# Kernel tuning notes

Measured on AMD Instinct MI355X. Metric: run time of the kernel, lower is better.

Reference implementation:

```python
import jax, jax.numpy as jnp
import numpy as np

B, T, I, H, O = 512, 1024, 15, 64, 11

def setup_inputs() -> dict:
    key = jax.random.key(0)
    ks = jax.random.split(key, 7)
    s_ih = 1.0 / np.sqrt(H)
    return {
        "x": jax.random.normal(ks[0], (B, T, I), dtype=jnp.float32),
        # torch nn.RNN params: weight_ih_l0 [H,I], weight_hh_l0 [H,H], biases [H]
        "W_ih": jax.random.uniform(ks[1], (H, I), jnp.float32, -s_ih, s_ih),
        "b_ih": jax.random.uniform(ks[2], (H,), jnp.float32, -s_ih, s_ih),
        "W_hh": jax.random.uniform(ks[3], (H, H), jnp.float32, -s_ih, s_ih),
        "b_hh": jax.random.uniform(ks[4], (H,), jnp.float32, -s_ih, s_ih),
        # decoder Linear(64, 11)
        "W_dec": jax.random.uniform(ks[5], (O, H), jnp.float32, -s_ih, s_ih),
        "b_dec": jax.random.uniform(ks[6], (O,), jnp.float32, -s_ih, s_ih),
    }

def reference(x, W_ih, b_ih, W_hh, b_hh, W_dec, b_dec):
    # Precompute input projection for all timesteps: [T, B, H]
    xproj = jnp.einsum("bti,hi->tbh", x, W_ih) + b_ih + b_hh
    h0 = jnp.zeros((x.shape[0], W_hh.shape[0]), dtype=x.dtype)

    def step(h, xp_t):
        h_new = jax.nn.relu(xp_t + h @ W_hh.T)  # [B, H]
        return h_new, h_new

    h_last, hs = jax.lax.scan(step, h0, xproj)  # hs: [T, B, H]
    out_seq = jnp.transpose(hs, (1, 0, 2))       # [B, T, H]
    out = jax.nn.relu(jnp.einsum("bth,oh->bto", out_seq, W_dec) + b_dec)
    h = h_last[None]  # [1, B, H] matching torch num_layers dim
    return (out, h)
```

## Files before the change

### kernel.cpp

```cpp
#include <hip/hip_runtime.h>
#include <hip/hip_fp16.h>
#include <stdint.h>

#define BB 512
#define TT 1024
#define II 15
#define HH 64
#define OO 11

typedef __fp16 half2v __attribute__((ext_vector_type(2)));
typedef _Float16 half8 __attribute__((ext_vector_type(8)));
typedef float floatx4 __attribute__((ext_vector_type(4)));
typedef int int4v __attribute__((ext_vector_type(4)));

union PK { int i; half2v h; float f; };

__device__ __forceinline__ half2v i2h2(int v) { PK u; u.i = v; return u.h; }
__device__ __forceinline__ int h22i(half2v v) { PK u; u.h = v; return u.i; }

__device__ __forceinline__ float FDOT2(half2v a, half2v b, float c) {
    return __builtin_amdgcn_fdot2(a, b, c, false);
}

__global__ __launch_bounds__(64) void rnn_rec(
    const float* __restrict__ x, const float* __restrict__ W_ih,
    const float* __restrict__ b_ih, const float* __restrict__ W_hh,
    const float* __restrict__ b_hh, _Float16* __restrict__ hs,
    float* __restrict__ h_last)
{
    __shared__ __align__(16) int xbuf[2][64 * 8];
    __shared__ __align__(16) _Float16 hbuf[64];
    const int b = blockIdx.x;
    const int lane = threadIdx.x;

    half2v whh[32];
#pragma unroll
    for (int p = 0; p < 32; ++p)
        whh[p] = __builtin_amdgcn_cvt_pkrtz(W_hh[lane * HH + 2 * p],
                                            W_hh[lane * HH + 2 * p + 1]);
    half2v wx[8];
#pragma unroll
    for (int j = 0; j < 7; ++j)
        wx[j] = __builtin_amdgcn_cvt_pkrtz(W_ih[lane * II + 2 * j],
                                           W_ih[lane * II + 2 * j + 1]);
    wx[7] = __builtin_amdgcn_cvt_pkrtz(W_ih[lane * II + 14],
                                       b_ih[lane] + b_hh[lane]);

    const float* xb = x + (size_t)b * TT * II;
    _Float16* hrow = hs + (size_t)b * TT * HH + lane;
    const int4v* hb4 = (const int4v*)hbuf;

    {
        float cf[II];
#pragma unroll
        for (int i = 0; i < II; ++i) cf[i] = xb[lane * II + i];
        int4v p0, p1;
        p0.x = h22i(__builtin_amdgcn_cvt_pkrtz(cf[0], cf[1]));
        p0.y = h22i(__builtin_amdgcn_cvt_pkrtz(cf[2], cf[3]));
        p0.z = h22i(__builtin_amdgcn_cvt_pkrtz(cf[4], cf[5]));
        p0.w = h22i(__builtin_amdgcn_cvt_pkrtz(cf[6], cf[7]));
        p1.x = h22i(__builtin_amdgcn_cvt_pkrtz(cf[8], cf[9]));
        p1.y = h22i(__builtin_amdgcn_cvt_pkrtz(cf[10], cf[11]));
        p1.z = h22i(__builtin_amdgcn_cvt_pkrtz(cf[12], cf[13]));
        p1.w = h22i(__builtin_amdgcn_cvt_pkrtz(cf[14], 1.0f));
        *(int4v*)&xbuf[0][lane * 8] = p0;
        *(int4v*)&xbuf[0][lane * 8 + 4] = p1;
    }
    hbuf[lane] = (_Float16)0.0f;

    float xa[8];
    {
        const int4v xv0 = *(const int4v*)&xbuf[0][0];
        const int4v xv1 = *(const int4v*)&xbuf[0][4];
        xa[0] = FDOT2(i2h2(xv0.x), wx[0], 0.0f);
        xa[1] = FDOT2(i2h2(xv0.y), wx[1], 0.0f);
        xa[2] = FDOT2(i2h2(xv0.z), wx[2], 0.0f);
        xa[3] = FDOT2(i2h2(xv0.w), wx[3], 0.0f);
        xa[4] = FDOT2(i2h2(xv1.x), wx[4], 0.0f);
        xa[5] = FDOT2(i2h2(xv1.y), wx[5], 0.0f);
        xa[6] = FDOT2(i2h2(xv1.z), wx[6], 0.0f);
        xa[7] = FDOT2(i2h2(xv1.w), wx[7], 0.0f);
    }

    float h = 0.0f;

    auto step = [&](int t) {
        int4v hb[8];
#pragma unroll
        for (int q = 0; q < 8; ++q) hb[q] = hb4[q];

        const int tn = t + 1;
        const int* xp = &xbuf[(tn >> 6) & 1][(tn & 63) * 8];
        const int4v xv0 = *(const int4v*)xp;
        const int4v xv1 = *(const int4v*)(xp + 4);

        float a0 = xa[0], a1 = xa[1], a2 = xa[2], a3 = xa[3];
        float a4 = xa[4], a5 = xa[5], a6 = xa[6], a7 = xa[7];
#pragma unroll
        for (int r = 0; r < 4; ++r) {
            a0 = FDOT2(i2h2(hb[2 * r].x),     whh[8 * r + 0], a0);
            a1 = FDOT2(i2h2(hb[2 * r].y),     whh[8 * r + 1], a1);
            a2 = FDOT2(i2h2(hb[2 * r].z),     whh[8 * r + 2], a2);
            a3 = FDOT2(i2h2(hb[2 * r].w),     whh[8 * r + 3], a3);
            a4 = FDOT2(i2h2(hb[2 * r + 1].x), whh[8 * r + 4], a4);
            a5 = FDOT2(i2h2(hb[2 * r + 1].y), whh[8 * r + 5], a5);
            a6 = FDOT2(i2h2(hb[2 * r + 1].z), whh[8 * r + 6], a6);
            a7 = FDOT2(i2h2(hb[2 * r + 1].w), whh[8 * r + 7], a7);
        }
        h = fmaxf(((a0 + a1) + (a2 + a3)) + ((a4 + a5) + (a6 + a7)), 0.0f);
        const _Float16 hf = (_Float16)h;
        hbuf[lane] = hf;
        hrow[(size_t)t * HH] = hf;

        xa[0] = FDOT2(i2h2(xv0.x), wx[0], 0.0f);
        xa[1] = FDOT2(i2h2(xv0.y), wx[1], 0.0f);
        xa[2] = FDOT2(i2h2(xv0.z), wx[2], 0.0f);
        xa[3] = FDOT2(i2h2(xv0.w), wx[3], 0.0f);
        xa[4] = FDOT2(i2h2(xv1.x), wx[4], 0.0f);
        xa[5] = FDOT2(i2h2(xv1.y), wx[5], 0.0f);
        xa[6] = FDOT2(i2h2(xv1.z), wx[6], 0.0f);
        xa[7] = FDOT2(i2h2(xv1.w), wx[7], 0.0f);
    };

    for (int tc = 0; tc < TT; tc += 64) {
        const int tnb = (tc + 64 < TT) ? (tc + 64) : tc;
        float nf[II];
#pragma unroll
        for (int i = 0; i < II; ++i)
            nf[i] = xb[(size_t)(tnb + lane) * II + i];

        for (int to = 0; to < 32; to += 8)
#pragma unroll
            for (int u = 0; u < 8; ++u) step(tc + to + u);

        {
            const int cb = ((tc >> 6) + 1) & 1;
            int4v p0, p1;
            p0.x = h22i(__builtin_amdgcn_cvt_pkrtz(nf[0], nf[1]));
            p0.y = h22i(__builtin_amdgcn_cvt_pkrtz(nf[2], nf[3]));
            p0.z = h22i(__builtin_amdgcn_cvt_pkrtz(nf[4], nf[5]));
            p0.w = h22i(__builtin_amdgcn_cvt_pkrtz(nf[6], nf[7]));
            p1.x = h22i(__builtin_amdgcn_cvt_pkrtz(nf[8], nf[9]));
            p1.y = h22i(__builtin_amdgcn_cvt_pkrtz(nf[10], nf[11]));
            p1.z = h22i(__builtin_amdgcn_cvt_pkrtz(nf[12], nf[13]));
            p1.w = h22i(__builtin_amdgcn_cvt_pkrtz(nf[14], 1.0f));
            *(int4v*)&xbuf[cb][lane * 8] = p0;
            *(int4v*)&xbuf[cb][lane * 8 + 4] = p1;
        }

        for (int to = 32; to < 64; to += 8)
#pragma unroll
            for (int u = 0; u < 8; ++u) step(tc + to + u);
    }
    h_last[b * HH + lane] = h;
}

__global__ __launch_bounds__(256) void rnn_decode(
    const _Float16* __restrict__ hs, const float* __restrict__ W_dec,
    const float* __restrict__ b_dec, float* __restrict__ out)
{
    __shared__ __align__(16) _Float16 wl[16 * HH];
    const int tid = threadIdx.x;
    for (int i = tid; i < 16 * HH; i += 256)
        wl[i] = (_Float16)((i < OO * HH) ? W_dec[i] : 0.0f);
    __syncthreads();

    const int lane = tid & 63;
    const int wid  = tid >> 6;
    const int col  = lane & 15;
    const int quad = lane >> 4;
    const float bd = (col < OO) ? b_dec[col] : 0.0f;

    half8 bf0 = *(const half8*)&wl[col * HH + quad * 8];
    half8 bf1 = *(const half8*)&wl[col * HH + 32 + quad * 8];

    const size_t tile = (size_t)blockIdx.x * 4 + wid;
    const size_t btb = tile * 16;
    const _Float16* ap = hs + (btb + (size_t)col) * HH + quad * 8;
    half8 a0 = *(const half8*)ap;
    half8 a1 = *(const half8*)(ap + 32);

    floatx4 acc = {0.0f, 0.0f, 0.0f, 0.0f};
    acc = __builtin_amdgcn_mfma_f32_16x16x32_f16(a0, bf0, acc, 0, 0, 0);
    acc = __builtin_amdgcn_mfma_f32_16x16x32_f16(a1, bf1, acc, 0, 0, 0);

    if (col < OO) {
#pragma unroll
        for (int r = 0; r < 4; ++r) {
            const size_t row = btb + (size_t)(quad * 4 + r);
            out[row * OO + col] = fmaxf(acc[r] + bd, 0.0f);
        }
    }
}

extern "C" void kernel_launch(void* const* d_in, const int* in_sizes, int n_in,
                              void* d_out, int out_size, void* d_ws, size_t ws_size,
                              hipStream_t stream) {
    const float* x     = (const float*)d_in[0];
    const float* W_ih  = (const float*)d_in[1];
    const float* b_ih  = (const float*)d_in[2];
    const float* W_hh  = (const float*)d_in[3];
    const float* b_hh  = (const float*)d_in[4];
    const float* W_dec = (const float*)d_in[5];
    const float* b_dec = (const float*)d_in[6];

    float* out    = (float*)d_out;
    float* h_last = out + (size_t)BB * TT * OO;
    _Float16* hs  = (_Float16*)d_ws;

    rnn_rec<<<BB, 64, 0, stream>>>(x, W_ih, b_ih, W_hh, b_hh, hs, h_last);
    rnn_decode<<<8192, 256, 0, stream>>>(hs, W_dec, b_dec, out);
}
```

Measured before the change: 273.8 us.

## Pack two batch rows per wavefront, each lane computing two hidden units

Each 64-lane block now handles two batch sequences: lanes 0-31 and 32-63 each own one batch, and every lane computes two hidden outputs with twice the recurrent weights held in registers. The grid is halved to 256 blocks, and hidden state is exchanged and stored as packed half2 words. This doubles per-lane serial work per step but halves the number of wavefronts, which suits a GPU with fewer CUs than 512 blocks, and it also doubles register pressure.

```diff
diff --git a/kernel.cpp b/kernel.cpp
--- a/kernel.cpp
+++ b/kernel.cpp
@@ -28,106 +28,143 @@
     const float* __restrict__ b_hh, _Float16* __restrict__ hs,
     float* __restrict__ h_last)
 {
-    __shared__ __align__(16) int xbuf[2][64 * 8];
-    __shared__ __align__(16) _Float16 hbuf[64];
-    const int b = blockIdx.x;
+    __shared__ __align__(16) int xbuf[2][2][64 * 8];
+    __shared__ __align__(16) int hbuf[64];
     const int lane = threadIdx.x;
-
-    half2v whh[32];
-#pragma unroll
-    for (int p = 0; p < 32; ++p)
-        whh[p] = __builtin_amdgcn_cvt_pkrtz(W_hh[lane * HH + 2 * p],
-                                            W_hh[lane * HH + 2 * p + 1]);
-    half2v wx[8];
-#pragma unroll
-    for (int j = 0; j < 7; ++j)
-        wx[j] = __builtin_amdgcn_cvt_pkrtz(W_ih[lane * II + 2 * j],
-                                           W_ih[lane * II + 2 * j + 1]);
-    wx[7] = __builtin_amdgcn_cvt_pkrtz(W_ih[lane * II + 14],
-                                       b_ih[lane] + b_hh[lane]);
-
-    const float* xb = x + (size_t)b * TT * II;
-    _Float16* hrow = hs + (size_t)b * TT * HH + lane;
-    const int4v* hb4 = (const int4v*)hbuf;
+    const int half = lane >> 5;
+    const int c = lane & 31;
+    const int b = blockIdx.x * 2 + half;
+    const int o0 = 2 * c, o1 = 2 * c + 1;
+
+    half2v wh0[32], wh1[32];
+#pragma unroll
+    for (int p = 0; p < 32; ++p) {
+        wh0[p] = __builtin_amdgcn_cvt_pkrtz(W_hh[o0 * HH + 2 * p],
+                                            W_hh[o0 * HH + 2 * p + 1]);
+        wh1[p] = __builtin_amdgcn_cvt_pkrtz(W_hh[o1 * HH + 2 * p],
+                                            W_hh[o1 * HH + 2 * p + 1]);
+    }
+    half2v wx0[8], wx1[8];
+#pragma unroll
+    for (int j = 0; j < 7; ++j) {
+        wx0[j] = __builtin_amdgcn_cvt_pkrtz(W_ih[o0 * II + 2 * j],
+                                            W_ih[o0 * II + 2 * j + 1]);
+        wx1[j] = __builtin_amdgcn_cvt_pkrtz(W_ih[o1 * II + 2 * j],
+                                            W_ih[o1 * II + 2 * j + 1]);
+    }
+    wx0[7] = __builtin_amdgcn_cvt_pkrtz(W_ih[o0 * II + 14],
+                                        b_ih[o0] + b_hh[o0]);
+    wx1[7] = __builtin_amdgcn_cvt_pkrtz(W_ih[o1 * II + 14],
+                                        b_ih[o1] + b_hh[o1]);
+
+    const float* xb0 = x + (size_t)(blockIdx.x * 2) * TT * II;
+    const float* xb1 = x + (size_t)(blockIdx.x * 2 + 1) * TT * II;
+    int* hrow = (int*)(hs + (size_t)b * TT * HH) + c;
 
     {
-        float cf[II];
-#pragma unroll
-        for (int i = 0; i < II; ++i) cf[i] = xb[lane * II + i];
-        int4v p0, p1;
-        p0.x = h22i(__builtin_amdgcn_cvt_pkrtz(cf[0], cf[1]));
-        p0.y = h22i(__builtin_amdgcn_cvt_pkrtz(cf[2], cf[3]));
-        p0.z = h22i(__builtin_amdgcn_cvt_pkrtz(cf[4], cf[5]));
-        p0.w = h22i(__builtin_amdgcn_cvt_pkrtz(cf[6], cf[7]));
-        p1.x = h22i(__builtin_amdgcn_cvt_pkrtz(cf[8], cf[9]));
-        p1.y = h22i(__builtin_amdgcn_cvt_pkrtz(cf[10], cf[11]));
-        p1.z = h22i(__builtin_amdgcn_cvt_pkrtz(cf[12], cf[13]));
-        p1.w = h22i(__builtin_amdgcn_cvt_pkrtz(cf[14], 1.0f));
-        *(int4v*)&xbuf[0][lane * 8] = p0;
-        *(int4v*)&xbuf[0][lane * 8 + 4] = p1;
-    }
-    hbuf[lane] = (_Float16)0.0f;
-
-    float xa[8];
+#pragma unroll
+        for (int q = 0; q < 2; ++q) {
+            const float* xq = q ? xb1 : xb0;
+            float cf[II];
+#pragma unroll
+            for (int i = 0; i < II; ++i) cf[i] = xq[lane * II + i];
+            int4v p0, p1;
+            p0.x = h22i(__builtin_amdgcn_cvt_pkrtz(cf[0], cf[1]));
+            p0.y = h22i(__builtin_amdgcn_cvt_pkrtz(cf[2], cf[3]));
+            p0.z = h22i(__builtin_amdgcn_cvt_pkrtz(cf[4], cf[5]));
+            p0.w = h22i(__builtin_amdgcn_cvt_pkrtz(cf[6], cf[7]));
+            p1.x = h22i(__builtin_amdgcn_cvt_pkrtz(cf[8], cf[9]));
+            p1.y = h22i(__builtin_amdgcn_cvt_pkrtz(cf[10], cf[11]));
+            p1.z = h22i(__builtin_amdgcn_cvt_pkrtz(cf[12], cf[13]));
+            p1.w = h22i(__builtin_amdgcn_cvt_pkrtz(cf[14], 1.0f));
+            *(int4v*)&xbuf[q][0][lane * 8] = p0;
+            *(int4v*)&xbuf[q][0][lane * 8 + 4] = p1;
+        }
+    }
+    hbuf[lane] = 0;
+
+    float xa0[4], xa1[4];
     {
-        const int4v xv0 = *(const int4v*)&xbuf[0][0];
-        const int4v xv1 = *(const int4v*)&xbuf[0][4];
-        xa[0] = FDOT2(i2h2(xv0.x), wx[0], 0.0f);
-        xa[1] = FDOT2(i2h2(xv0.y), wx[1], 0.0f);
-        xa[2] = FDOT2(i2h2(xv0.z), wx[2], 0.0f);
-        xa[3] = FDOT2(i2h2(xv0.w), wx[3], 0.0f);
-        xa[4] = FDOT2(i2h2(xv1.x), wx[4], 0.0f);
-        xa[5] = FDOT2(i2h2(xv1.y), wx[5], 0.0f);
-        xa[6] = FDOT2(i2h2(xv1.z), wx[6], 0.0f);
-        xa[7] = FDOT2(i2h2(xv1.w), wx[7], 0.0f);
-    }
-
-    float h = 0.0f;
+        const int4v xv0 = *(const int4v*)&xbuf[half][0][0];
+        const int4v xv1 = *(const int4v*)&xbuf[half][0][4];
+        xa0[0] = FDOT2(i2h2(xv0.x), wx0[0], 0.0f);
+        xa0[1] = FDOT2(i2h2(xv0.y), wx0[1], 0.0f);
+        xa0[2] = FDOT2(i2h2(xv0.z), wx0[2], 0.0f);
+        xa0[3] = FDOT2(i2h2(xv0.w), wx0[3], 0.0f);
+        xa0[0] = FDOT2(i2h2(xv1.x), wx0[4], xa0[0]);
+        xa0[1] = FDOT2(i2h2(xv1.y), wx0[5], xa0[1]);
+        xa0[2] = FDOT2(i2h2(xv1.z), wx0[6], xa0[2]);
+        xa0[3] = FDOT2(i2h2(xv1.w), wx0[7], xa0[3]);
+        xa1[0] = FDOT2(i2h2(xv0.x), wx1[0], 0.0f);
+        xa1[1] = FDOT2(i2h2(xv0.y), wx1[1], 0.0f);
+        xa1[2] = FDOT2(i2h2(xv0.z), wx1[2], 0.0f);
+        xa1[3] = FDOT2(i2h2(xv0.w), wx1[3], 0.0f);
+        xa1[0] = FDOT2(i2h2(xv1.x), wx1[4], xa1[0]);
+        xa1[1] = FDOT2(i2h2(xv1.y), wx1[5], xa1[1]);
+        xa1[2] = FDOT2(i2h2(xv1.z), wx1[6], xa1[2]);
+        xa1[3] = FDOT2(i2h2(xv1.w), wx1[7], xa1[3]);
+    }
+
+    float h0 = 0.0f, h1 = 0.0f;
 
     auto step = [&](int t) {
         int4v hb[8];
 #pragma unroll
-        for (int q = 0; q < 8; ++q) hb[q] = hb4[q];
+        for (int q = 0; q < 8; ++q)
+            hb[q] = *(const int4v*)&hbuf[half * 32 + q * 4];
+
+        float A0 = xa0[0], A1 = xa0[1], A2 = xa0[2], A3 = xa0[3];
+        float B0 = xa1[0], B1 = xa1[1], B2 = xa1[2], B3 = xa1[3];
+#pragma unroll
+        for (int q = 0; q < 8; ++q) {
+            A0 = FDOT2(i2h2(hb[q].x), wh0[4 * q + 0], A0);
+            A1 = FDOT2(i2h2(hb[q].y), wh0[4 * q + 1], A1);
+            A2 = FDOT2(i2h2(hb[q].z), wh0[4 * q + 2], A2);
+            A3 = FDOT2(i2h2(hb[q].w), wh0[4 * q + 3], A3);
+            B0 = FDOT2(i2h2(hb[q].x), wh1[4 * q + 0], B0);
+            B1 = FDOT2(i2h2(hb[q].y), wh1[4 * q + 1], B1);
+            B2 = FDOT2(i2h2(hb[q].z), wh1[4 * q + 2], B2);
+            B3 = FDOT2(i2h2(hb[q].w), wh1[4 * q + 3], B3);
+        }
+        h0 = fmaxf((A0 + A1) + (A2 + A3), 0.0f);
+        h1 = fmaxf((B0 + B1) + (B2 + B3), 0.0f);
+        const int pk = h22i(__builtin_amdgcn_cvt_pkrtz(h0, h1));
+        hbuf[half * 32 + c] = pk;
 
         const int tn = t + 1;
-        const int* xp = &xbuf[(tn >> 6) & 1][(tn & 63) * 8];
+        const int* xp = &xbuf[half][(tn >> 6) & 1][(tn & 63) * 8];
         const int4v xv0 = *(const int4v*)xp;
         const int4v xv1 = *(const int4v*)(xp + 4);
 
-        float a0 = xa[0], a1 = xa[1], a2 = xa[2], a3 = xa[3];
-        float a4 = xa[4], a5 = xa[5], a6 = xa[6], a7 = xa[7];
-#pragma unroll
-        for (int r = 0; r < 4; ++r) {
-            a0 = FDOT2(i2h2(hb[2 * r].x),     whh[8 * r + 0], a0);
-            a1 = FDOT2(i2h2(hb[2 * r].y),     whh[8 * r + 1], a1);
-            a2 = FDOT2(i2h2(hb[2 * r].z),     whh[8 * r + 2], a2);
-            a3 = FDOT2(i2h2(hb[2 * r].w),     whh[8 * r + 3], a3);
-            a4 = FDOT2(i2h2(hb[2 * r + 1].x), whh[8 * r + 4], a4);
-            a5 = FDOT2(i2h2(hb[2 * r + 1].y), whh[8 * r + 5], a5);
-            a6 = FDOT2(i2h2(hb[2 * r + 1].z), whh[8 * r + 6], a6);
-            a7 = FDOT2(i2h2(hb[2 * r + 1].w), whh[8 * r + 7], a7);
-        }
-        h = fmaxf(((a0 + a1) + (a2 + a3)) + ((a4 + a5) + (a6 + a7)), 0.0f);
-        const _Float16 hf = (_Float16)h;
-        hbuf[lane] = hf;
-        hrow[(size_t)t * HH] = hf;
-
-        xa[0] = FDOT2(i2h2(xv0.x), wx[0], 0.0f);
-        xa[1] = FDOT2(i2h2(xv0.y), wx[1], 0.0f);
-        xa[2] = FDOT2(i2h2(xv0.z), wx[2], 0.0f);
-        xa[3] = FDOT2(i2h2(xv0.w), wx[3], 0.0f);
-        xa[4] = FDOT2(i2h2(xv1.x), wx[4], 0.0f);
-        xa[5] = FDOT2(i2h2(xv1.y), wx[5], 0.0f);
-        xa[6] = FDOT2(i2h2(xv1.z), wx[6], 0.0f);
-        xa[7] = FDOT2(i2h2(xv1.w), wx[7], 0.0f);
+        hrow[(size_t)t * 32] = pk;
+
+        xa0[0] = FDOT2(i2h2(xv0.x), wx0[0], 0.0f);
+        xa0[1] = FDOT2(i2h2(xv0.y), wx0[1], 0.0f);
+        xa0[2] = FDOT2(i2h2(xv0.z), wx0[2], 0.0f);
+        xa0[3] = FDOT2(i2h2(xv0.w), wx0[3], 0.0f);
+        xa0[0] = FDOT2(i2h2(xv1.x), wx0[4], xa0[0]);
+        xa0[1] = FDOT2(i2h2(xv1.y), wx0[5], xa0[1]);
+        xa0[2] = FDOT2(i2h2(xv1.z), wx0[6], xa0[2]);
+        xa0[3] = FDOT2(i2h2(xv1.w), wx0[7], xa0[3]);
+        xa1[0] = FDOT2(i2h2(xv0.x), wx1[0], 0.0f);
+        xa1[1] = FDOT2(i2h2(xv0.y), wx1[1], 0.0f);
+        xa1[2] = FDOT2(i2h2(xv0.z), wx1[2], 0.0f);
+        xa1[3] = FDOT2(i2h2(xv0.w), wx1[3], 0.0f);
+        xa1[0] = FDOT2(i2h2(xv1.x), wx1[4], xa1[0]);
+        xa1[1] = FDOT2(i2h2(xv1.y), wx1[5], xa1[1]);
+        xa1[2] = FDOT2(i2h2(xv1.z), wx1[6], xa1[2]);
+        xa1[3] = FDOT2(i2h2(xv1.w), wx1[7], xa1[3]);
     };
 
     for (int tc = 0; tc < TT; tc += 64) {
         const int tnb = (tc + 64 < TT) ? (tc + 64) : tc;
-        float nf[II];
+        float nf0[II], nf1[II];
 #pragma unroll
         for (int i = 0; i < II; ++i)
-            nf[i] = xb[(size_t)(tnb + lane) * II + i];
+            nf0[i] = xb0[(size_t)(tnb + lane) * II + i];
+#pragma unroll
+        for (int i = 0; i < II; ++i)
+            nf1[i] = xb1[(size_t)(tnb + lane) * II + i];
 
         for (int to = 0; to < 32; to += 8)
 #pragma unroll
@@ -135,24 +172,29 @@
 
         {
             const int cb = ((tc >> 6) + 1) & 1;
-            int4v p0, p1;
-            p0.x = h22i(__builtin_amdgcn_cvt_pkrtz(nf[0], nf[1]));
-            p0.y = h22i(__builtin_amdgcn_cvt_pkrtz(nf[2], nf[3]));
-            p0.z = h22i(__builtin_amdgcn_cvt_pkrtz(nf[4], nf[5]));
-            p0.w = h22i(__builtin_amdgcn_cvt_pkrtz(nf[6], nf[7]));
-            p1.x = h22i(__builtin_amdgcn_cvt_pkrtz(nf[8], nf[9]));
-            p1.y = h22i(__builtin_amdgcn_cvt_pkrtz(nf[10], nf[11]));
-            p1.z = h22i(__builtin_amdgcn_cvt_pkrtz(nf[12], nf[13]));
-            p1.w = h22i(__builtin_amdgcn_cvt_pkrtz(nf[14], 1.0f));
-            *(int4v*)&xbuf[cb][lane * 8] = p0;
-            *(int4v*)&xbuf[cb][lane * 8 + 4] = p1;
+#pragma unroll
+            for (int q = 0; q < 2; ++q) {
+                const float* nf = q ? nf1 : nf0;
+                int4v p0, p1;
+                p0.x = h22i(__builtin_amdgcn_cvt_pkrtz(nf[0], nf[1]));
+                p0.y = h22i(__builtin_amdgcn_cvt_pkrtz(nf[2], nf[3]));
+                p0.z = h22i(__builtin_amdgcn_cvt_pkrtz(nf[4], nf[5]));
+                p0.w = h22i(__builtin_amdgcn_cvt_pkrtz(nf[6], nf[7]));
+                p1.x = h22i(__builtin_amdgcn_cvt_pkrtz(nf[8], nf[9]));
+                p1.y = h22i(__builtin_amdgcn_cvt_pkrtz(nf[10], nf[11]));
+                p1.z = h22i(__builtin_amdgcn_cvt_pkrtz(nf[12], nf[13]));
+                p1.w = h22i(__builtin_amdgcn_cvt_pkrtz(nf[14], 1.0f));
+                *(int4v*)&xbuf[q][cb][lane * 8] = p0;
+                *(int4v*)&xbuf[q][cb][lane * 8 + 4] = p1;
+            }
         }
 
         for (int to = 32; to < 64; to += 8)
 #pragma unroll
             for (int u = 0; u < 8; ++u) step(tc + to + u);
     }
-    h_last[b * HH + lane] = h;
+    h_last[(size_t)b * HH + o0] = h0;
+    h_last[(size_t)b * HH + o1] = h1;
 }
 
 __global__ __launch_bounds__(256) void rnn_decode(
@@ -208,6 +250,6 @@
     float* h_last = out + (size_t)BB * TT * OO;
     _Float16* hs  = (_Float16*)d_ws;
 
-    rnn_rec<<<BB, 64, 0, stream>>>(x, W_ih, b_ih, W_hh, b_hh, hs, h_last);
+    rnn_rec<<<BB / 2, 64, 0, stream>>>(x, W_ih, b_ih, W_hh, b_hh, hs, h_last);
     rnn_decode<<<8192, 256, 0, stream>>>(hs, W_dec, b_dec, out);
 }
```

New measurement: 346.3 us. 1.26x slower.

## Interleave two batch recurrences per wavefront to hide step latency

Applied to the files above, without the earlier changes.

Each 64-lane block now advances two independent batch rows in lockstep, alternating phases of the recurrence so that one row's LDS round-trip and dot-product chain overlaps with the other's. The grid is halved so that each wave carries two recurrences instead of one. The input-projection dot products move to the start of each phase, and the h reload is issued right after the write. In exchange it uses more registers per wave and fewer waves in total, so latency hiding now relies on interleaving within a wave rather than across waves.

```diff
diff --git a/kernel.cpp b/kernel.cpp
--- a/kernel.cpp
+++ b/kernel.cpp
@@ -28,10 +28,10 @@
     const float* __restrict__ b_hh, _Float16* __restrict__ hs,
     float* __restrict__ h_last)
 {
-    __shared__ __align__(16) int xbuf[2][64 * 8];
-    __shared__ __align__(16) _Float16 hbuf[64];
-    const int b = blockIdx.x;
+    __shared__ __align__(16) int xbuf[2][2][64 * 8];
+    __shared__ __align__(16) _Float16 hbuf[2][64];
     const int lane = threadIdx.x;
+    const int b0 = blockIdx.x * 2;
 
     half2v whh[32];
 #pragma unroll
@@ -46,14 +46,17 @@
     wx[7] = __builtin_amdgcn_cvt_pkrtz(W_ih[lane * II + 14],
                                        b_ih[lane] + b_hh[lane]);
 
-    const float* xb = x + (size_t)b * TT * II;
-    _Float16* hrow = hs + (size_t)b * TT * HH + lane;
-    const int4v* hb4 = (const int4v*)hbuf;
-
-    {
+    const float* xb0 = x + (size_t)b0 * TT * II;
+    const float* xb1 = x + (size_t)(b0 + 1) * TT * II;
+    _Float16* hr0 = hs + (size_t)b0 * TT * HH + lane;
+    _Float16* hr1 = hs + (size_t)(b0 + 1) * TT * HH + lane;
+
+#pragma unroll
+    for (int q = 0; q < 2; ++q) {
+        const float* xq = q ? xb1 : xb0;
         float cf[II];
 #pragma unroll
-        for (int i = 0; i < II; ++i) cf[i] = xb[lane * II + i];
+        for (int i = 0; i < II; ++i) cf[i] = xq[lane * II + i];
         int4v p0, p1;
         p0.x = h22i(__builtin_amdgcn_cvt_pkrtz(cf[0], cf[1]));
         p0.y = h22i(__builtin_amdgcn_cvt_pkrtz(cf[2], cf[3]));
@@ -63,39 +66,34 @@
         p1.y = h22i(__builtin_amdgcn_cvt_pkrtz(cf[10], cf[11]));
         p1.z = h22i(__builtin_amdgcn_cvt_pkrtz(cf[12], cf[13]));
         p1.w = h22i(__builtin_amdgcn_cvt_pkrtz(cf[14], 1.0f));
-        *(int4v*)&xbuf[0][lane * 8] = p0;
-        *(int4v*)&xbuf[0][lane * 8 + 4] = p1;
+        *(int4v*)&xbuf[q][0][lane * 8] = p0;
+        *(int4v*)&xbuf[q][0][lane * 8 + 4] = p1;
     }
-    hbuf[lane] = (_Float16)0.0f;
-
-    float xa[8];
-    {
-        const int4v xv0 = *(const int4v*)&xbuf[0][0];
-        const int4v xv1 = *(const int4v*)&xbuf[0][4];
-        xa[0] = FDOT2(i2h2(xv0.x), wx[0], 0.0f);
-        xa[1] = FDOT2(i2h2(xv0.y), wx[1], 0.0f);
-        xa[2] = FDOT2(i2h2(xv0.z), wx[2], 0.0f);
-        xa[3] = FDOT2(i2h2(xv0.w), wx[3], 0.0f);
-        xa[4] = FDOT2(i2h2(xv1.x), wx[4], 0.0f);
-        xa[5] = FDOT2(i2h2(xv1.y), wx[5], 0.0f);
-        xa[6] = FDOT2(i2h2(xv1.z), wx[6], 0.0f);
-        xa[7] = FDOT2(i2h2(xv1.w), wx[7], 0.0f);
-    }
-
-    float h = 0.0f;
-
-    auto step = [&](int t) {
-        int4v hb[8];
-#pragma unroll
-        for (int q = 0; q < 8; ++q) hb[q] = hb4[q];
-
-        const int tn = t + 1;
-        const int* xp = &xbuf[(tn >> 6) & 1][(tn & 63) * 8];
-        const int4v xv0 = *(const int4v*)xp;
-        const int4v xv1 = *(const int4v*)(xp + 4);
-
-        float a0 = xa[0], a1 = xa[1], a2 = xa[2], a3 = xa[3];
-        float a4 = xa[4], a5 = xa[5], a6 = xa[6], a7 = xa[7];
+    hbuf[0][lane] = (_Float16)0.0f;
+    hbuf[1][lane] = (_Float16)0.0f;
+
+    int4v hbA[8], hbB[8], xvA0, xvA1, xvB0, xvB1;
+#pragma unroll
+    for (int i = 0; i < 8; ++i) hbA[i] = ((const int4v*)hbuf[0])[i];
+    xvA0 = *(const int4v*)&xbuf[0][0][0];
+    xvA1 = *(const int4v*)&xbuf[0][0][4];
+#pragma unroll
+    for (int i = 0; i < 8; ++i) hbB[i] = ((const int4v*)hbuf[1])[i];
+    xvB0 = *(const int4v*)&xbuf[1][0][0];
+    xvB1 = *(const int4v*)&xbuf[1][0][4];
+
+    float hA = 0.0f, hB = 0.0f;
+
+    auto phase = [&](int q, int4v (&hb)[8], int4v& xv0, int4v& xv1,
+                     float& h, _Float16* hr, int t) {
+        float a0 = FDOT2(i2h2(xv0.x), wx[0], 0.0f);
+        float a1 = FDOT2(i2h2(xv0.y), wx[1], 0.0f);
+        float a2 = FDOT2(i2h2(xv0.z), wx[2], 0.0f);
+        float a3 = FDOT2(i2h2(xv0.w), wx[3], 0.0f);
+        float a4 = FDOT2(i2h2(xv1.x), wx[4], 0.0f);
+        float a5 = FDOT2(i2h2(xv1.y), wx[5], 0.0f);
+        float a6 = FDOT2(i2h2(xv1.z), wx[6], 0.0f);
+        float a7 = FDOT2(i2h2(xv1.w), wx[7], 0.0f);
 #pragma unroll
         for (int r = 0; r < 4; ++r) {
             a0 = FDOT2(i2h2(hb[2 * r].x),     whh[8 * r + 0], a0);
@@ -109,50 +107,63 @@
         }
         h = fmaxf(((a0 + a1) + (a2 + a3)) + ((a4 + a5) + (a6 + a7)), 0.0f);
         const _Float16 hf = (_Float16)h;
-        hbuf[lane] = hf;
-        hrow[(size_t)t * HH] = hf;
-
-        xa[0] = FDOT2(i2h2(xv0.x), wx[0], 0.0f);
-        xa[1] = FDOT2(i2h2(xv0.y), wx[1], 0.0f);
-        xa[2] = FDOT2(i2h2(xv0.z), wx[2], 0.0f);
-        xa[3] = FDOT2(i2h2(xv0.w), wx[3], 0.0f);
-        xa[4] = FDOT2(i2h2(xv1.x), wx[4], 0.0f);
-        xa[5] = FDOT2(i2h2(xv1.y), wx[5], 0.0f);
-        xa[6] = FDOT2(i2h2(xv1.z), wx[6], 0.0f);
-        xa[7] = FDOT2(i2h2(xv1.w), wx[7], 0.0f);
+        hbuf[q][lane] = hf;
+#pragma unroll
+        for (int i = 0; i < 8; ++i) hb[i] = ((const int4v*)hbuf[q])[i];
+        const int tn = t + 1;
+        const int* xp = &xbuf[q][(tn >> 6) & 1][(tn & 63) * 8];
+        xv0 = *(const int4v*)xp;
+        xv1 = *(const int4v*)(xp + 4);
+        hr[(size_t)t * HH] = hf;
     };
 
     for (int tc = 0; tc < TT; tc += 64) {
         const int tnb = (tc + 64 < TT) ? (tc + 64) : tc;
-        float nf[II];
+        float nf0[II], nf1[II];
 #pragma unroll
         for (int i = 0; i < II; ++i)
-            nf[i] = xb[(size_t)(tnb + lane) * II + i];
-
-        for (int to = 0; to < 32; to += 8)
-#pragma unroll
-            for (int u = 0; u < 8; ++u) step(tc + to + u);
+            nf0[i] = xb0[(size_t)(tnb + lane) * II + i];
+#pragma unroll
+        for (int i = 0; i < II; ++i)
+            nf1[i] = xb1[(size_t)(tnb + lane) * II + i];
+
+        for (int to = 0; to < 32; to += 4)
+#pragma unroll
+            for (int u = 0; u < 4; ++u) {
+                const int t = tc + to + u;
+                phase(0, hbA, xvA0, xvA1, hA, hr0, t);
+                phase(1, hbB, xvB0, xvB1, hB, hr1, t);
+            }
 
         {
             const int cb = ((tc >> 6) + 1) & 1;
-            int4v p0, p1;
-            p0.x = h22i(__builtin_amdgcn_cvt_pkrtz(nf[0], nf[1]));
-            p0.y = h22i(__builtin_amdgcn_cvt_pkrtz(nf[2], nf[3]));
-            p0.z = h22i(__builtin_amdgcn_cvt_pkrtz(nf[4], nf[5]));
-            p0.w = h22i(__builtin_amdgcn_cvt_pkrtz(nf[6], nf[7]));
-            p1.x = h22i(__builtin_amdgcn_cvt_pkrtz(nf[8], nf[9]));
-            p1.y = h22i(__builtin_amdgcn_cvt_pkrtz(nf[10], nf[11]));
-            p1.z = h22i(__builtin_amdgcn_cvt_pkrtz(nf[12], nf[13]));
-            p1.w = h22i(__builtin_amdgcn_cvt_pkrtz(nf[14], 1.0f));
-            *(int4v*)&xbuf[cb][lane * 8] = p0;
-            *(int4v*)&xbuf[cb][lane * 8 + 4] = p1;
+#pragma unroll
+            for (int q = 0; q < 2; ++q) {
+                const float* nf = q ? nf1 : nf0;
+                int4v p0, p1;
+                p0.x = h22i(__builtin_amdgcn_cvt_pkrtz(nf[0], nf[1]));
+                p0.y = h22i(__builtin_amdgcn_cvt_pkrtz(nf[2], nf[3]));
+                p0.z = h22i(__builtin_amdgcn_cvt_pkrtz(nf[4], nf[5]));
+                p0.w = h22i(__builtin_amdgcn_cvt_pkrtz(nf[6], nf[7]));
+                p1.x = h22i(__builtin_amdgcn_cvt_pkrtz(nf[8], nf[9]));
+                p1.y = h22i(__builtin_amdgcn_cvt_pkrtz(nf[10], nf[11]));
+                p1.z = h22i(__builtin_amdgcn_cvt_pkrtz(nf[12], nf[13]));
+                p1.w = h22i(__builtin_amdgcn_cvt_pkrtz(nf[14], 1.0f));
+                *(int4v*)&xbuf[q][cb][lane * 8] = p0;
+                *(int4v*)&xbuf[q][cb][lane * 8 + 4] = p1;
+            }
         }
 
-        for (int to = 32; to < 64; to += 8)
-#pragma unroll
-            for (int u = 0; u < 8; ++u) step(tc + to + u);
+        for (int to = 32; to < 64; to += 4)
+#pragma unroll
+            for (int u = 0; u < 4; ++u) {
+                const int t = tc + to + u;
+                phase(0, hbA, xvA0, xvA1, hA, hr0, t);
+                phase(1, hbB, xvB0, xvB1, hB, hr1, t);
+            }
     }
-    h_last[b * HH + lane] = h;
+    h_last[(size_t)b0 * HH + lane] = hA;
+    h_last[(size_t)(b0 + 1) * HH + lane] = hB;
 }
 
 __global__ __launch_bounds__(256) void rnn_decode(
@@ -208,6 +219,6 @@
     float* h_last = out + (size_t)BB * TT * OO;
     _Float16* hs  = (_Float16*)d_ws;
 
-    rnn_rec<<<BB, 64, 0, stream>>>(x, W_ih, b_ih, W_hh, b_hh, hs, h_last);
+    rnn_rec<<<BB / 2, 64, 0, stream>>>(x, W_ih, b_ih, W_hh, b_hh, hs, h_last);
     rnn_decode<<<8192, 256, 0, stream>>>(hs, W_dec, b_dec, out);
 }
```

New measurement: 382.3 us. 1.4x slower.
